# Kernel optimization log

Measured on AMD Instinct MI355X. Metric: run time of the kernel, lower is better.

## Reference

```python
import jax, jax.numpy as jnp
import numpy as np

NC = 10          # tess_size (number of tessellation cells on [0,1])
D = NC - 1       # CPA parameter dim with zero boundary
EPS = 1e-7
N = 2097152      # number of 2D points
MASK = jnp.array([1, 0])  # left=True coupling mask

def _make_basis(nc):
    # Continuous piecewise-affine velocity on [0,1]: cell c has v(x)=a_c*x+b_c.
    # Constraints: continuity at interior knots + zero boundary v(0)=v(1)=0.
    L = np.zeros((nc + 1, 2 * nc))
    for k in range(1, nc):
        xk = k / nc
        L[k - 1, 2 * (k - 1)] = xk; L[k - 1, 2 * (k - 1) + 1] = 1.0
        L[k - 1, 2 * k] = -xk;      L[k - 1, 2 * k + 1] = -1.0
    L[nc - 1, 1] = 1.0                                        # v(0) = 0
    L[nc, 2 * (nc - 1)] = 1.0; L[nc, 2 * (nc - 1) + 1] = 1.0  # v(1) = 0
    _, _, Vt = np.linalg.svd(L)
    return jnp.asarray(Vt[nc + 1:].T, dtype=jnp.float32)      # (2*nc, D) null-space basis (svd)

_B = _make_basis(NC)

def cpab_flow(x, theta):
    """Integrate dphi/dt = v(phi), t in [0,1], v CPA parameterized by theta.
    x: (N,1) in [0,1], theta: (N,D). Returns (phi(x,1), dphi/dx), each (N,1).
    Closed-form per-cell integration with cell hopping (<= NC hops, fixed scan).
    dphi/dx = exp(sum_c a_c * dt_c) (analytic space gradient)."""
    A = (theta @ _B.T).reshape(-1, NC, 2)          # (N, NC, 2): (a_c, b_c)
    xp = x[:, 0]
    c0 = jnp.clip((xp * NC).astype(jnp.int32), 0, NC - 1)
    carry0 = (xp, jnp.ones_like(xp), c0, jnp.zeros_like(xp))

    def step(carry, _):
        phi, t, c, ld = carry
        a = jnp.take_along_axis(A[:, :, 0], c[:, None], 1)[:, 0]
        b = jnp.take_along_axis(A[:, :, 1], c[:, None], 1)[:, 0]
        v = a * phi + b
        lin = jnp.abs(a) < 1e-10
        sa = jnp.where(lin, 1.0, a)
        xc = jnp.where(v >= 0, (c + 1).astype(phi.dtype), c.astype(phi.dtype)) / NC
        den = phi + b / sa
        den = jnp.where(jnp.abs(den) < 1e-30, 1e-30, den)
        t_exp = jnp.log(jnp.maximum((xc + b / sa) / den, 1e-30)) / sa
        sb = jnp.where(jnp.abs(b) < 1e-30, 1.0, b)
        thit = jnp.where(lin, (xc - phi) / sb, t_exp)
        thit = jnp.where(jnp.abs(v) < 1e-14, jnp.inf, thit)   # fixed point: never leaves cell
        cross = thit < t
        dt = jnp.where(cross, thit, t)
        phi_new = jnp.where(lin, phi + b * dt,
                            (phi + b / sa) * jnp.exp(a * dt) - b / sa)
        phi_new = jnp.where(cross, xc, phi_new)               # snap to knot when hopping
        active = t > 0
        phi = jnp.where(active, phi_new, phi)
        ld = ld + jnp.where(active, a * dt, 0.0)              # accumulate log dphi/dx
        t = jnp.where(active, t - dt, t)
        c = jnp.where(active & cross,
                      jnp.clip(c + jnp.where(v >= 0, 1, -1), 0, NC - 1), c)
        return (phi, t, c, ld), None

    (phi, _, _, ld), _ = jax.lax.scan(step, carry0, None, length=NC)
    return phi[:, None], jnp.exp(ld)[:, None]

def mlp(h, p):
    # Linear -> (Linear, ReLU) x 2 -> Linear  (matches torch MLP(hidden_layers=3))
    h = h @ p[0] + p[1]
    h = jax.nn.relu(h @ p[2] + p[3])
    h = jax.nn.relu(h @ p[4] + p[5])
    return h @ p[6] + p[7]

def setup_inputs():
    key = jax.random.key(0)
    ks = jax.random.split(key, 17)
    inp = {"x": jax.random.uniform(ks[0], (N, 2), dtype=jnp.float32)}
    shapes = [(1, 10), (10,), (10, 10), (10,), (10, 10), (10,), (10, D), (D,)]
    names = ["w0", "b0", "w1", "b1", "w2", "b2", "w3", "b3"]
    i = 1
    for pref in ("m1", "m2"):
        for nm, sh in zip(names, shapes):
            scale = 0.3 if len(sh) == 2 else 0.1
            inp[pref + nm] = jax.random.normal(ks[i], sh, dtype=jnp.float32) * scale
            i += 1
    return inp

def reference(x, m1w0, m1b0, m1w1, m1b1, m1w2, m1b2, m1w3, m1b3,
              m2w0, m2b0, m2w1, m2b1, m2w2, m2b2, m2w3, m2b3):
    x = jnp.clip(x, EPS, 1.0 - EPS)
    xs = x[:, MASK]                        # index_select with coupling mask
    x1, x2 = xs[:, 0:1], xs[:, 1:2]
    theta2 = mlp(x1, (m2w0, m2b0, m2w1, m2b1, m2w2, m2b2, m2w3, m2b3))
    z2, g2 = cpab_flow(x2, theta2)
    theta1 = mlp(z2, (m1w0, m1b0, m1w1, m1b1, m1w2, m1b2, m1w3, m1b3))
    z1, g1 = cpab_flow(x1, theta1)
    z = jnp.concatenate([z1, z2], axis=1)[:, MASK]
    log_dz_dx = jnp.log(jnp.concatenate([g1, g2], axis=1))[:, MASK]
    return z, log_dz_dx
```

## Files before the change

kernel.cpp:

```cpp
#include <hip/hip_runtime.h>
#include <cmath>

#define THREADS 256
#define NCELL 10
#define DDIM 9

typedef float f32x2 __attribute__((ext_vector_type(2)));

__device__ __forceinline__ f32x2 fma2(f32x2 a, f32x2 b, f32x2 c) {
  return __builtin_elementwise_fma(a, b, c);
}
__device__ __forceinline__ f32x2 max2(f32x2 a, f32x2 b) {
  return __builtin_elementwise_max(a, b);
}

struct Basis { float Bt[DDIM][2 * NCELL]; };

static void compute_basis_host(Basis* bs) {
  double L[11][20];
  for (int r = 0; r < 11; ++r)
    for (int c = 0; c < 20; ++c) L[r][c] = 0.0;
  for (int k = 1; k < NCELL; ++k) {
    double xk = (double)k / (double)NCELL;
    L[k - 1][2 * (k - 1)] = xk;
    L[k - 1][2 * (k - 1) + 1] = 1.0;
    L[k - 1][2 * k] = -xk;
    L[k - 1][2 * k + 1] = -1.0;
  }
  L[NCELL - 1][1] = 1.0;
  L[NCELL][2 * (NCELL - 1)] = 1.0;
  L[NCELL][2 * (NCELL - 1) + 1] = 1.0;

  double v[11][20];
  double tau[11];
  for (int i = 0; i < 11; ++i) {
    double alpha = L[i][i];
    double xn2 = 0.0;
    for (int l = i + 1; l < 20; ++l) xn2 += L[i][l] * L[i][l];
    double xnorm = sqrt(xn2);
    for (int l = 0; l < 20; ++l) v[i][l] = 0.0;
    v[i][i] = 1.0;
    if (xnorm == 0.0) {
      tau[i] = 0.0;
    } else {
      double beta = sqrt(alpha * alpha + xn2);
      if (alpha >= 0.0) beta = -beta;
      tau[i] = (beta - alpha) / beta;
      double sc = 1.0 / (alpha - beta);
      for (int l = i + 1; l < 20; ++l) v[i][l] = L[i][l] * sc;
      L[i][i] = beta;
      for (int j = i + 1; j < 11; ++j) {
        double w = 0.0;
        for (int l = i; l < 20; ++l) w += L[j][l] * v[i][l];
        w *= tau[i];
        for (int l = i; l < 20; ++l) L[j][l] -= w * v[i][l];
      }
    }
  }
  for (int j = 11; j < 20; ++j) {
    double q[20];
    for (int l = 0; l < 20; ++l) q[l] = 0.0;
    q[j] = 1.0;
    for (int i = 10; i >= 0; --i) {
      double w = 0.0;
      for (int l = i; l < 20; ++l) w += v[i][l] * q[l];
      w *= tau[i];
      for (int l = i; l < 20; ++l) q[l] -= w * v[i][l];
    }
    for (int l = 0; l < 20; ++l) bs->Bt[j - 11][l] = (float)q[l];
  }
}

__global__ void fold_kernel(
    const float* __restrict__ w0_1, const float* __restrict__ b0_1,
    const float* __restrict__ w1_1, const float* __restrict__ b1_1,
    const float* __restrict__ w3_1, const float* __restrict__ b3_1,
    const float* __restrict__ w0_2, const float* __restrict__ b0_2,
    const float* __restrict__ w1_2, const float* __restrict__ b1_2,
    const float* __restrict__ w3_2, const float* __restrict__ b3_2,
    float* __restrict__ ws, Basis bb) {
  for (int f = threadIdx.x; f < 480; f += THREADS) {
    int m = f / 240;
    int j = f % 240;
    const float* w0 = (m == 0) ? w0_1 : w0_2;
    const float* b0 = (m == 0) ? b0_1 : b0_2;
    const float* w1 = (m == 0) ? w1_1 : w1_2;
    const float* b1 = (m == 0) ? b1_1 : b1_2;
    const float* w3 = (m == 0) ? w3_1 : w3_2;
    const float* b3 = (m == 0) ? b3_1 : b3_2;
    float val = 0.0f;
    if (j < 10) {
      for (int r = 0; r < 10; ++r) val += w0[r] * w1[r * 10 + j];
    } else if (j < 20) {
      int jj = j - 10;
      for (int r = 0; r < 10; ++r) val += b0[r] * w1[r * 10 + jj];
      val += b1[jj];
    } else if (j < 220) {
      int jj = j - 20;
      int r = jj / 20, l = jj % 20;
      for (int t = 0; t < DDIM; ++t) val += w3[r * DDIM + t] * bb.Bt[t][l];
    } else {
      int l = j - 220;
      for (int t = 0; t < DDIM; ++t) val += b3[t] * bb.Bt[t][l];
    }
    ws[f] = val;
  }
}

__device__ __forceinline__ void mlp_A(float xin,
    const float* __restrict__ w2, const float* __restrict__ b2,
    const float* __restrict__ wbf,
    f32x2* abcol, float& amin) {
  const f32x2* W01 = (const f32x2*)wbf;
  const f32x2* B01 = W01 + 5;
  const f32x2* W3B = W01 + 10;
  const f32x2* B3B = W01 + 110;
  const f32x2* w2p = (const f32x2*)w2;
  const f32x2* b2p = (const f32x2*)b2;

  f32x2 h1[5], h2[5];
  f32x2 xx = {xin, xin};
  f32x2 zero = {0.0f, 0.0f};
#pragma unroll
  for (int p = 0; p < 5; ++p) h1[p] = max2(fma2(xx, W01[p], B01[p]), zero);

#pragma unroll
  for (int p = 0; p < 5; ++p) h2[p] = b2p[p];
#pragma unroll
  for (int r = 0; r < 10; ++r) {
    float h = h1[r >> 1][r & 1];
    f32x2 hh = {h, h};
#pragma unroll
    for (int p = 0; p < 5; ++p) h2[p] = fma2(hh, w2p[r * 5 + p], h2[p]);
  }
#pragma unroll
  for (int p = 0; p < 5; ++p) h2[p] = max2(h2[p], zero);

  f32x2 acc[NCELL];
#pragma unroll
  for (int l = 0; l < NCELL; ++l) acc[l] = B3B[l];
#pragma unroll
  for (int r = 0; r < 10; ++r) {
    float h = h2[r >> 1][r & 1];
    f32x2 hh = {h, h};
#pragma unroll
    for (int l = 0; l < NCELL; ++l) acc[l] = fma2(hh, W3B[r * 10 + l], acc[l]);
  }
  float mn = 1e30f;
#pragma unroll
  for (int l = 0; l < NCELL; ++l) {
    abcol[l * THREADS] = acc[l];
    mn = fminf(mn, fabsf(acc[l][0]));
  }
  amin = mn;
}

__device__ __forceinline__ void flow_dev(float x0, const f32x2* abcol,
                                         bool has_lin, float& zo, float& ldo) {
  int c = (int)(x0 * 10.0f);
  c = c < 0 ? 0 : (c > 9 ? 9 : c);
  f32x2 ab = abcol[c * THREADS];
  float a = ab[0], b = ab[1];
  float v0 = fmaf(a, x0, b);
  bool right = (v0 >= 0.0f);
  float d01 = right ? 0.1f : -0.1f;
  int dirI = right ? 1 : -1;
  float xc = (float)(right ? (c + 1) : c) * 0.1f;
  float rv0 = __builtin_amdgcn_rcpf(v0);
  float rv = rv0;
  float vcur = v0;
  bool tiny = fabsf(v0) < 1e-14f;
  float ra = __builtin_amdgcn_rcpf(a);
  float phiC = x0;
  float t = 1.0f;
  float trem = 0.0f;

  int cn = c + dirI; cn = cn < 0 ? 0 : (cn > 9 ? 9 : cn);
  f32x2 abn = abcol[cn * THREADS];
  float ran = __builtin_amdgcn_rcpf(abn[0]);

  for (int it = 0; it < NCELL; ++it) {
    float vxc = fmaf(a, xc, b);
    float ratio = fmaxf(vxc * rv, 1e-30f);
    float l = __logf(ratio);
    float thit = l * ra;
    if (has_lin) {
      bool lin = fabsf(a) < 1e-10f;
      float sb = (fabsf(b) < 1e-30f) ? 1.0f : b;
      float tl = (xc - phiC) * __builtin_amdgcn_rcpf(sb);
      thit = lin ? tl : thit;
    }
    bool active = t > 0.0f;
    bool cross = (thit < t) && !tiny;
    bool ac = active && cross;
    bool term = active && !cross;
    trem = term ? t : trem;
    float tn = t - thit;
    t = active ? (cross ? tn : 0.0f) : t;
    phiC = ac ? xc : phiC;
    vcur = ac ? vxc : vcur;
    float rvn = __builtin_amdgcn_rcpf(vxc);
    rv = ac ? rvn : rv;
    tiny = ac ? (fabsf(vxc) < 1e-14f) : tiny;
    a = ac ? abn[0] : a;
    b = ac ? abn[1] : b;
    ra = ac ? ran : ra;
    xc = ac ? (xc + d01) : xc;
    c = ac ? cn : c;
    if (__all(t <= 0.0f)) break;
    int cnn = c + dirI; cnn = cnn < 0 ? 0 : (cnn > 9 ? 9 : cnn);
    abn = abcol[cnn * THREADS];
    ran = __builtin_amdgcn_rcpf(abn[0]);
    cn = cnn;
  }
  bool done = trem > 0.0f;
  float ld = __logf(fmaxf(vcur * rv0, 1e-30f));
  bool linf = fabsf(a) < 1e-10f;
  float rsaf = __builtin_amdgcn_rcpf(linf ? 1.0f : a);
  float bsa = b * rsaf;
  float E = __expf(a * trem);
  float pnl = fmaf(phiC + bsa, E, -bsa);
  float pli = fmaf(b, trem, phiC);
  float p1 = linf ? pli : pnl;
  zo = done ? p1 : phiC;
  ldo = ld + (done ? a * trem : 0.0f);
}

__global__ __launch_bounds__(THREADS, 4) void cpab2d_kernel(
    const float* __restrict__ x,
    const float* __restrict__ m1w2, const float* __restrict__ m1b2,
    const float* __restrict__ m2w2, const float* __restrict__ m2b2,
    const float* __restrict__ wsf,
    float* __restrict__ out, int n) {
  __shared__ f32x2 AB[NCELL][THREADS];
  int i = blockIdx.x * THREADS + threadIdx.x;
  if (i >= n) return;

  float2 xi = reinterpret_cast<const float2*>(x)[i];
  float x2v = fminf(fmaxf(xi.x, 1e-7f), 1.0f - 1e-7f);
  float x1v = fminf(fmaxf(xi.y, 1e-7f), 1.0f - 1e-7f);

  f32x2* abcol = &AB[0][threadIdx.x];
  float amin;

  mlp_A(x1v, m2w2, m2b2, wsf + 240, abcol, amin);
  bool hl2 = __any(amin < 1e-10f);
  float z2, ld2;
  flow_dev(x2v, abcol, hl2, z2, ld2);

  mlp_A(z2, m1w2, m1b2, wsf, abcol, amin);
  bool hl1 = __any(amin < 1e-10f);
  float z1, ld1;
  flow_dev(x1v, abcol, hl1, z1, ld1);

  reinterpret_cast<float2*>(out)[i] = make_float2(z2, z1);
  reinterpret_cast<float2*>(out + 2 * (size_t)n)[i] = make_float2(ld2, ld1);
}

extern "C" void kernel_launch(void* const* d_in, const int* in_sizes, int n_in,
                              void* d_out, int out_size, void* d_ws, size_t ws_size,
                              hipStream_t stream) {
  const float* x    = (const float*)d_in[0];
  const float* m1w0 = (const float*)d_in[1];
  const float* m1b0 = (const float*)d_in[2];
  const float* m1w1 = (const float*)d_in[3];
  const float* m1b1 = (const float*)d_in[4];
  const float* m1w2 = (const float*)d_in[5];
  const float* m1b2 = (const float*)d_in[6];
  const float* m1w3 = (const float*)d_in[7];
  const float* m1b3 = (const float*)d_in[8];
  const float* m2w0 = (const float*)d_in[9];
  const float* m2b0 = (const float*)d_in[10];
  const float* m2w1 = (const float*)d_in[11];
  const float* m2b1 = (const float*)d_in[12];
  const float* m2w2 = (const float*)d_in[13];
  const float* m2b2 = (const float*)d_in[14];
  const float* m2w3 = (const float*)d_in[15];
  const float* m2b3 = (const float*)d_in[16];
  float* out = (float*)d_out;
  float* wsf = (float*)d_ws;
  int n = in_sizes[0] / 2;

  Basis bs;
  compute_basis_host(&bs);

  fold_kernel<<<1, THREADS, 0, stream>>>(
      m1w0, m1b0, m1w1, m1b1, m1w3, m1b3,
      m2w0, m2b0, m2w1, m2b1, m2w3, m2b3, wsf, bs);

  dim3 grid((n + THREADS - 1) / THREADS), block(THREADS);
  cpab2d_kernel<<<grid, block, 0, stream>>>(
      x, m1w2, m1b2, m2w2, m2b2, wsf, out, n);
}
```

Before: 51.22 us.

## Project MLP output to knot velocities and derive cell slopes from differences

The final MLP layer now folds the CPA basis into 9 interior knot velocities instead of 20 per-cell (a,b) coefficients, halving the last-layer FMAs. Per-cell slope and intercept are then rebuilt from adjacent knot-velocity differences. The flow loop is also simplified: the active and terminal bookkeeping is replaced by a single cross flag, and the terminal velocity is recomputed at the end. This relies on the basis being exactly continuous and zero at the boundaries, which can shift floating-point rounding slightly compared with the reference.

```diff
diff --git a/kernel.cpp b/kernel.cpp
--- a/kernel.cpp
+++ b/kernel.cpp
@@ -79,15 +79,15 @@
     const float* __restrict__ w1_2, const float* __restrict__ b1_2,
     const float* __restrict__ w3_2, const float* __restrict__ b3_2,
     float* __restrict__ ws, Basis bb) {
-  for (int f = threadIdx.x; f < 480; f += THREADS) {
-    int m = f / 240;
-    int j = f % 240;
+  for (int f = threadIdx.x; f < 260; f += THREADS) {
+    int m = f / 130;
+    int j = f % 130;
     const float* w0 = (m == 0) ? w0_1 : w0_2;
     const float* b0 = (m == 0) ? b0_1 : b0_2;
     const float* w1 = (m == 0) ? w1_1 : w1_2;
-    const float* b1 = (m == 0) ? b1_1 : b1_2;
     const float* w3 = (m == 0) ? w3_1 : w3_2;
     const float* b3 = (m == 0) ? b3_1 : b3_2;
+    const float* b1 = (m == 0) ? b1_1 : b1_2;
     float val = 0.0f;
     if (j < 10) {
       for (int r = 0; r < 10; ++r) val += w0[r] * w1[r * 10 + j];
@@ -95,13 +95,21 @@
       int jj = j - 10;
       for (int r = 0; r < 10; ++r) val += b0[r] * w1[r * 10 + jj];
       val += b1[jj];
-    } else if (j < 220) {
+    } else if (j < 120) {
       int jj = j - 20;
-      int r = jj / 20, l = jj % 20;
-      for (int t = 0; t < DDIM; ++t) val += w3[r * DDIM + t] * bb.Bt[t][l];
+      int r = jj / 10, k = jj % 10;
+      if (k < 9) {
+        float g = (float)(k + 1) * 0.1f;
+        for (int t = 0; t < DDIM; ++t)
+          val += w3[r * DDIM + t] * (bb.Bt[t][2 * (k + 1)] * g + bb.Bt[t][2 * (k + 1) + 1]);
+      }
     } else {
-      int l = j - 220;
-      for (int t = 0; t < DDIM; ++t) val += b3[t] * bb.Bt[t][l];
+      int k = j - 120;
+      if (k < 9) {
+        float g = (float)(k + 1) * 0.1f;
+        for (int t = 0; t < DDIM; ++t)
+          val += b3[t] * (bb.Bt[t][2 * (k + 1)] * g + bb.Bt[t][2 * (k + 1) + 1]);
+      }
     }
     ws[f] = val;
   }
@@ -113,8 +121,8 @@
     f32x2* abcol, float& amin) {
   const f32x2* W01 = (const f32x2*)wbf;
   const f32x2* B01 = W01 + 5;
-  const f32x2* W3B = W01 + 10;
-  const f32x2* B3B = W01 + 110;
+  const f32x2* W3V = W01 + 10;
+  const f32x2* B3V = W01 + 60;
   const f32x2* w2p = (const f32x2*)w2;
   const f32x2* b2p = (const f32x2*)b2;
 
@@ -136,21 +144,30 @@
 #pragma unroll
   for (int p = 0; p < 5; ++p) h2[p] = max2(h2[p], zero);
 
-  f32x2 acc[NCELL];
-#pragma unroll
-  for (int l = 0; l < NCELL; ++l) acc[l] = B3B[l];
+  f32x2 vp[5];
+#pragma unroll
+  for (int p = 0; p < 5; ++p) vp[p] = B3V[p];
 #pragma unroll
   for (int r = 0; r < 10; ++r) {
     float h = h2[r >> 1][r & 1];
     f32x2 hh = {h, h};
 #pragma unroll
-    for (int l = 0; l < NCELL; ++l) acc[l] = fma2(hh, W3B[r * 10 + l], acc[l]);
-  }
+    for (int p = 0; p < 5; ++p) vp[p] = fma2(hh, W3V[r * 5 + p], vp[p]);
+  }
+
+  float v[NCELL + 1];
+  v[0] = 0.0f;
+#pragma unroll
+  for (int k = 1; k <= NCELL; ++k) v[k] = vp[(k - 1) >> 1][(k - 1) & 1];
+
   float mn = 1e30f;
 #pragma unroll
-  for (int l = 0; l < NCELL; ++l) {
-    abcol[l * THREADS] = acc[l];
-    mn = fminf(mn, fabsf(acc[l][0]));
+  for (int c = 0; c < NCELL; ++c) {
+    float ac = (v[c + 1] - v[c]) * 10.0f;
+    float bc = fmaf(ac, -(float)c * 0.1f, v[c]);
+    f32x2 ab; ab[0] = ac; ab[1] = bc;
+    abcol[c * THREADS] = ab;
+    mn = fminf(mn, fabsf(ac));
   }
   amin = mn;
 }
@@ -168,12 +185,11 @@
   float xc = (float)(right ? (c + 1) : c) * 0.1f;
   float rv0 = __builtin_amdgcn_rcpf(v0);
   float rv = rv0;
-  float vcur = v0;
   bool tiny = fabsf(v0) < 1e-14f;
   float ra = __builtin_amdgcn_rcpf(a);
   float phiC = x0;
   float t = 1.0f;
-  float trem = 0.0f;
+  bool cross = false;
 
   int cn = c + dirI; cn = cn < 0 ? 0 : (cn > 9 ? 9 : cn);
   f32x2 abn = abcol[cn * THREADS];
@@ -190,40 +206,35 @@
       float tl = (xc - phiC) * __builtin_amdgcn_rcpf(sb);
       thit = lin ? tl : thit;
     }
-    bool active = t > 0.0f;
-    bool cross = (thit < t) && !tiny;
-    bool ac = active && cross;
-    bool term = active && !cross;
-    trem = term ? t : trem;
-    float tn = t - thit;
-    t = active ? (cross ? tn : 0.0f) : t;
-    phiC = ac ? xc : phiC;
-    vcur = ac ? vxc : vcur;
+    cross = (thit < t) && !tiny;
+    t = cross ? (t - thit) : t;
+    phiC = cross ? xc : phiC;
     float rvn = __builtin_amdgcn_rcpf(vxc);
-    rv = ac ? rvn : rv;
-    tiny = ac ? (fabsf(vxc) < 1e-14f) : tiny;
-    a = ac ? abn[0] : a;
-    b = ac ? abn[1] : b;
-    ra = ac ? ran : ra;
-    xc = ac ? (xc + d01) : xc;
-    c = ac ? cn : c;
-    if (__all(t <= 0.0f)) break;
+    rv = cross ? rvn : rv;
+    tiny = cross ? (fabsf(vxc) < 1e-14f) : tiny;
+    a = cross ? abn[0] : a;
+    b = cross ? abn[1] : b;
+    ra = cross ? ran : ra;
+    xc = cross ? (xc + d01) : xc;
+    c = cross ? cn : c;
+    if (__all(!cross)) break;
     int cnn = c + dirI; cnn = cnn < 0 ? 0 : (cnn > 9 ? 9 : cnn);
     abn = abcol[cnn * THREADS];
     ran = __builtin_amdgcn_rcpf(abn[0]);
     cn = cnn;
   }
-  bool done = trem > 0.0f;
-  float ld = __logf(fmaxf(vcur * rv0, 1e-30f));
+  bool done = !cross;
+  float vterm = fmaf(a, phiC, b);
+  float ld = __logf(fmaxf(vterm * rv0, 1e-30f));
   bool linf = fabsf(a) < 1e-10f;
   float rsaf = __builtin_amdgcn_rcpf(linf ? 1.0f : a);
   float bsa = b * rsaf;
-  float E = __expf(a * trem);
+  float E = __expf(a * t);
   float pnl = fmaf(phiC + bsa, E, -bsa);
-  float pli = fmaf(b, trem, phiC);
+  float pli = fmaf(b, t, phiC);
   float p1 = linf ? pli : pnl;
   zo = done ? p1 : phiC;
-  ldo = ld + (done ? a * trem : 0.0f);
+  ldo = ld + (done ? a * t : 0.0f);
 }
 
 __global__ __launch_bounds__(THREADS, 4) void cpab2d_kernel(
@@ -243,7 +254,7 @@
   f32x2* abcol = &AB[0][threadIdx.x];
   float amin;
 
-  mlp_A(x1v, m2w2, m2b2, wsf + 240, abcol, amin);
+  mlp_A(x1v, m2w2, m2b2, wsf + 130, abcol, amin);
   bool hl2 = __any(amin < 1e-10f);
   float z2, ld2;
   flow_dev(x2v, abcol, hl2, z2, ld2);
```

Result: faster. 45.82 us (-10.5%).
